# Kernel optimization log

Measured on AMD Instinct MI355X. Metric: run time of the kernel, lower is better.

The kernel has to match this reference:

```python
import jax, jax.numpy as jnp
import numpy as np

N_NODES = 100000
N_EDGES = 3200000
IN_CH = 128
HID_CH = 128   # 2 * out_channels
OUT_CH = 64


def setup_inputs() -> dict:
    key = jax.random.key(0)
    ks = jax.random.split(key, 6)
    x = jax.random.normal(ks[0], (N_NODES, IN_CH), dtype=jnp.float32)
    edge_index = jax.random.randint(ks[1], (2, N_EDGES), 0, N_NODES, dtype=jnp.int64)
    # Glorot-ish init for GCN linear weights
    W1 = jax.random.normal(ks[2], (IN_CH, HID_CH), dtype=jnp.float32) / np.sqrt(IN_CH)
    b1 = jnp.zeros((HID_CH,), dtype=jnp.float32)
    W2 = jax.random.normal(ks[3], (HID_CH, OUT_CH), dtype=jnp.float32) / np.sqrt(HID_CH)
    b2 = jnp.zeros((OUT_CH,), dtype=jnp.float32)
    return {"x": x, "edge_index": edge_index, "W1": W1, "b1": b1, "W2": W2, "b2": b2}


def gcn_conv(x, src, dst, W, b, n):
    """PyG GCNConv: add self-loops, symmetric D^-1/2 (A+I) D^-1/2 normalization,
    linear transform, scatter-add aggregation, then bias."""
    h = x @ W  # [N, C_out]
    ones = jnp.ones(src.shape[0], dtype=x.dtype)
    deg = jax.ops.segment_sum(ones, dst, num_segments=n) + 1.0  # self-loop degree
    dinv = jax.lax.rsqrt(deg)  # [N]
    coef = dinv[src] * dinv[dst]  # [E] edge normalization
    agg = jax.ops.segment_sum(h[src] * coef[:, None], dst, num_segments=n)
    agg = agg + h * (dinv * dinv)[:, None]  # self-loop contribution
    return agg + b


def reference(x, edge_index, W1, b1, W2, b2):
    src, dst = edge_index[0], edge_index[1]
    n = x.shape[0]
    h = jax.nn.relu(gcn_conv(x, src, dst, W1, b1, n))
    out = jax.nn.relu(gcn_conv(h, src, dst, W2, b2, n))
    return out
```

## Files before the change

kernel.cpp:

```cpp
#include <hip/hip_runtime.h>
#include <hip/hip_fp16.h>
#include <cstdint>
#include <cstddef>


#define BSHIFT 8
#define CAP    12288

typedef _Float16 half8 __attribute__((ext_vector_type(8)));
typedef float f32x4 __attribute__((ext_vector_type(4)));

__global__ __launch_bounds__(256) void k_binit(int* __restrict__ bktcur, int nbkt) {
  int b = blockIdx.x * 256 + threadIdx.x;
  if (b < nbkt) bktcur[b] = b * CAP;
}

__global__ __launch_bounds__(256) void k_part3(const int* __restrict__ src,
                                               const int* __restrict__ dst,
                                               int* __restrict__ bktcur,
                                               int* __restrict__ part, int E,
                                               int nbkt) {
  __shared__ int vals[4096];
  __shared__ unsigned short bid[4096];
  __shared__ int hist[512];
  __shared__ int lbase[512];
  __shared__ int gbase[512];
  const int tid = threadIdx.x;
  const int e0 = blockIdx.x * 4096;
  const int ecnt = min(4096, E - e0);
  for (int b = tid; b < nbkt; b += 256) hist[b] = 0;
  __syncthreads();

  int eb[16], ev[16];
#pragma unroll
  for (int j = 0; j < 16; ++j) {
    const int e = e0 + j * 256 + tid;
    eb[j] = -1;
    ev[j] = 0;
    if (e < E) {
      const int d = dst[e];
      eb[j] = d >> BSHIFT;
      ev[j] = (src[e] << BSHIFT) | (d & ((1 << BSHIFT) - 1));
      atomicAdd(&hist[eb[j]], 1);
    }
  }
  __syncthreads();

  if (tid == 0) {
    int run = 0;
    for (int b = 0; b < nbkt; ++b) {
      const int c = hist[b];
      lbase[b] = run;
      run += c;
    }
  }
  __syncthreads();
  for (int b = tid; b < nbkt; b += 256) {
    const int c = hist[b];
    gbase[b] = c ? atomicAdd(&bktcur[b], c) : 0;
    hist[b] = lbase[b];
  }
  __syncthreads();

#pragma unroll
  for (int j = 0; j < 16; ++j) {
    if (eb[j] >= 0) {
      const int lpos = atomicAdd(&hist[eb[j]], 1);
      vals[lpos] = ev[j];
      bid[lpos] = (unsigned short)eb[j];
    }
  }
  __syncthreads();

  for (int s = tid; s < ecnt; s += 256) {
    const int b = bid[s];
    const int gpos = gbase[b] + (s - lbase[b]);
    if (gpos < (b + 1) * CAP)
      part[gpos] = vals[s];
  }
}

__global__ __launch_bounds__(256) void k_bktscan(const int* __restrict__ bktcur,
                                                 int* __restrict__ bktbase,
                                                 int* __restrict__ offsets, int n,
                                                 int E, int nbkt) {
  __shared__ int sc[512];
  const int t = threadIdx.x;
  sc[t] = (t < nbkt) ? (bktcur[t] - t * CAP) : 0;
  sc[256 + t] = (256 + t < nbkt) ? (bktcur[256 + t] - (256 + t) * CAP) : 0;
  __syncthreads();
  if (t == 0) {
    int run = 0;
    for (int b = 0; b < nbkt; ++b) {
      const int c = sc[b];
      sc[b] = run;
      run += c;
    }
    offsets[n] = E;
    bktbase[nbkt] = E;
  }
  __syncthreads();
  if (t < nbkt) bktbase[t] = sc[t];
  if (256 + t < nbkt) bktbase[256 + t] = sc[256 + t];
}

__global__ __launch_bounds__(256) void k_csr2(const int* __restrict__ part,
                                              const int* __restrict__ bktcur,
                                              const int* __restrict__ bktbase,
                                              int* __restrict__ offsets,
                                              int* __restrict__ csr_src,
                                              float* __restrict__ dinv, int n) {
  __shared__ int cnt[256];
  __shared__ int ts[256];
  const int b = blockIdx.x;
  const int node0 = b << BSHIFT;
  const int nn = min(256, n - node0);
  const int t = threadIdx.x;
  cnt[t] = 0;
  __syncthreads();
  const int w0p = b * CAP;
  const int w1p = min(bktcur[b], w0p + CAP);
  for (int e = w0p + t; e < w1p; e += 256)
    atomicAdd(&cnt[part[e] & ((1 << BSHIFT) - 1)], 1);
  __syncthreads();
  const int c = cnt[t];
  ts[t] = c;
  __syncthreads();
  for (int off = 1; off < 256; off <<= 1) {
    const int u = (t >= off) ? ts[t - off] : 0;
    __syncthreads();
    ts[t] += u;
    __syncthreads();
  }
  const int excl = ts[t] - c;
  const int w0 = bktbase[b];
  if (t < nn) {
    offsets[node0 + t] = w0 + excl;
    dinv[node0 + t] = rsqrtf((float)c + 1.0f);
  }
  cnt[t] = w0 + excl;
  __syncthreads();
  for (int e = w0p + t; e < w1p; e += 256) {
    const int p = part[e];
    const int pos = atomicAdd(&cnt[p & ((1 << BSHIFT) - 1)], 1);
    csr_src[pos] = p >> BSHIFT;
  }
}

template <typename TA, int COLS>
__global__ __launch_bounds__(256) void k_gemm_mfma(const TA* __restrict__ A,
                                                   const float* __restrict__ W,
                                                   const float* __restrict__ dinv,
                                                   __half* __restrict__ Hout,
                                                   int N, int ntiles) {
  constexpr int RW = (COLS == 128) ? 2 : 4;
  constexpr int RPT = RW * 16;
  __shared__ _Float16 Wt[128 * COLS];
  __shared__ _Float16 Lb[4][16][72];
  const int tid = threadIdx.x;
  const int w = tid >> 6;
  const int l = tid & 63;

  for (int f = tid; f < (128 * COLS) / 4; f += 256) {
    const int k = f / (COLS / 4);
    const int c4 = (f % (COLS / 4)) * 4;
    const float4 wv = *reinterpret_cast<const float4*>(W + (size_t)k * COLS + c4);
#pragma unroll
    for (int j = 0; j < 4; ++j) {
      const int cc = c4 + j;
      Wt[(cc * 128 + k) ^ ((cc & 7) << 3)] = (_Float16)(&wv.x)[j];
    }
  }
  __syncthreads();

  const int colw = (COLS == 128) ? (w >> 1) * 64 : 0;
  const int rw = (COLS == 128) ? (w & 1) : w;
  const int koff = (l >> 4) * 8;

  half8 bf[4][4];
#pragma unroll
  for (int t = 0; t < 4; ++t)
#pragma unroll
    for (int s = 0; s < 4; ++s) {
      const int cc = colw + 16 * t + (l & 15);
      const int kk = 32 * s + koff;
      bf[t][s] =
          *reinterpret_cast<const half8*>(&Wt[(cc * 128 + kk) ^ ((cc & 7) << 3)]);
    }

  for (int tile = blockIdx.x; tile < ntiles; tile += gridDim.x) {
    const int row = tile * RPT + rw * 16 + (l & 15);
    const int rowc = (row < N) ? row : (N - 1);
    f32x4 acc[4];
#pragma unroll
    for (int t = 0; t < 4; ++t) acc[t] = (f32x4){0.f, 0.f, 0.f, 0.f};

#pragma unroll
    for (int s = 0; s < 4; ++s) {
      half8 af;
      if constexpr (sizeof(TA) == 4) {
        const float* ap = (const float*)A + (size_t)rowc * 128 + 32 * s + koff;
        const float4 a0 = *reinterpret_cast<const float4*>(ap);
        const float4 a1 = *reinterpret_cast<const float4*>(ap + 4);
#pragma unroll
        for (int j = 0; j < 4; ++j) {
          af[j] = (_Float16)(&a0.x)[j];
          af[4 + j] = (_Float16)(&a1.x)[j];
        }
      } else {
        af = *reinterpret_cast<const half8*>((const __half*)A +
                                             (size_t)rowc * 128 + 32 * s + koff);
      }
#pragma unroll
      for (int t = 0; t < 4; ++t)
        acc[t] = __builtin_amdgcn_mfma_f32_16x16x32_f16(af, bf[t][s], acc[t],
                                                        0, 0, 0);
    }

    const int rbase = tile * RPT + rw * 16 + (l >> 4) * 4;
    float dr[4];
#pragma unroll
    for (int r = 0; r < 4; ++r) {
      const int rr = rbase + r;
      dr[r] = (rr < N) ? dinv[rr] : 0.f;
    }

#pragma unroll
    for (int t = 0; t < 4; ++t)
#pragma unroll
      for (int r = 0; r < 4; ++r)
        Lb[w][(l >> 4) * 4 + r][16 * t + (l & 15)] = (_Float16)(acc[t][r] * dr[r]);
    const int orow = tile * RPT + rw * 16 + (l & 15);
    if (orow < N) {
      const int ch = (l >> 4) * 16;
      const half8 v0 = *reinterpret_cast<const half8*>(&Lb[w][l & 15][ch]);
      const half8 v1 = *reinterpret_cast<const half8*>(&Lb[w][l & 15][ch + 8]);
      __half* hp = Hout + (size_t)orow * COLS + colw + ch;
      *reinterpret_cast<half8*>(hp) = v0;
      *reinterpret_cast<half8*>(hp + 8) = v1;
    }
  }
}

__global__ __launch_bounds__(256) void k_gather128(
    const __half* __restrict__ H, const int* __restrict__ offsets,
    const int* __restrict__ csr_src, const float* __restrict__ dinv,
    const float* __restrict__ bias, __half* __restrict__ out, int N) {
  const int lane = threadIdx.x & 63;
  const int g = lane >> 3;
  const int sl = lane & 7;
  int w = (blockIdx.x * 256 + threadIdx.x) >> 6;
  const int nw = (gridDim.x * 256) >> 6;
  for (int i = w; i < N; i += nw) {
    const int beg = offsets[i];
    const int end = offsets[i + 1];
    float acc[16];
    {
      const float vf = (g == 0) ? 1.f : 0.f;
      const float4 ha = *reinterpret_cast<const float4*>(H + (size_t)i * 128 + sl * 16);
      const float4 hb = *reinterpret_cast<const float4*>(H + (size_t)i * 128 + sl * 16 + 8);
      const __half2* pa = reinterpret_cast<const __half2*>(&ha);
      const __half2* pb = reinterpret_cast<const __half2*>(&hb);
#pragma unroll
      for (int q = 0; q < 4; ++q) {
        const float2 fa = __half22float2(pa[q]);
        const float2 fb = __half22float2(pb[q]);
        acc[q * 2] = vf * fa.x;
        acc[q * 2 + 1] = vf * fa.y;
        acc[8 + q * 2] = vf * fb.x;
        acc[8 + q * 2 + 1] = vf * fb.y;
      }
    }
    int base = beg;
    for (; base + 16 <= end; base += 16) {
      const int s0 = __builtin_nontemporal_load(csr_src + base + g);
      const int s1 = __builtin_nontemporal_load(csr_src + base + 8 + g);
      const float4 h0a = *reinterpret_cast<const float4*>(H + (size_t)s0 * 128 + sl * 16);
      const float4 h0b = *reinterpret_cast<const float4*>(H + (size_t)s0 * 128 + sl * 16 + 8);
      const float4 h1a = *reinterpret_cast<const float4*>(H + (size_t)s1 * 128 + sl * 16);
      const float4 h1b = *reinterpret_cast<const float4*>(H + (size_t)s1 * 128 + sl * 16 + 8);
      const __half2* p0a = reinterpret_cast<const __half2*>(&h0a);
      const __half2* p0b = reinterpret_cast<const __half2*>(&h0b);
      const __half2* p1a = reinterpret_cast<const __half2*>(&h1a);
      const __half2* p1b = reinterpret_cast<const __half2*>(&h1b);
#pragma unroll
      for (int q = 0; q < 4; ++q) {
        const float2 f0a = __half22float2(p0a[q]);
        const float2 f0b = __half22float2(p0b[q]);
        const float2 f1a = __half22float2(p1a[q]);
        const float2 f1b = __half22float2(p1b[q]);
        acc[q * 2] += f0a.x + f1a.x;
        acc[q * 2 + 1] += f0a.y + f1a.y;
        acc[8 + q * 2] += f0b.x + f1b.x;
        acc[8 + q * 2 + 1] += f0b.y + f1b.y;
      }
    }
    for (; base < end; base += 8) {
      const int e = base + g;
      const bool v = e < end;
      const int s = v ? __builtin_nontemporal_load(csr_src + e) : i;
      const float vf = v ? 1.f : 0.f;
      const float4 ha = *reinterpret_cast<const float4*>(H + (size_t)s * 128 + sl * 16);
      const float4 hb = *reinterpret_cast<const float4*>(H + (size_t)s * 128 + sl * 16 + 8);
      const __half2* pa = reinterpret_cast<const __half2*>(&ha);
      const __half2* pb = reinterpret_cast<const __half2*>(&hb);
#pragma unroll
      for (int q = 0; q < 4; ++q) {
        const float2 fa = __half22float2(pa[q]);
        const float2 fb = __half22float2(pb[q]);
        acc[q * 2] = fmaf(vf, fa.x, acc[q * 2]);
        acc[q * 2 + 1] = fmaf(vf, fa.y, acc[q * 2 + 1]);
        acc[8 + q * 2] = fmaf(vf, fb.x, acc[8 + q * 2]);
        acc[8 + q * 2 + 1] = fmaf(vf, fb.y, acc[8 + q * 2 + 1]);
      }
    }
#pragma unroll
    for (int j = 0; j < 16; ++j) {
      float a = acc[j];
      a += __shfl_xor(a, 8);
      a += __shfl_xor(a, 16);
      a += __shfl_xor(a, 32);
      acc[j] = a;
    }
    if (g == 0) {
      const float di = dinv[i];
      __half2 ov[8];
#pragma unroll
      for (int q = 0; q < 8; ++q) {
        const float2 bv = *reinterpret_cast<const float2*>(bias + sl * 16 + q * 2);
        ov[q] = __floats2half2_rn(fmaxf(fmaf(di, acc[q * 2], bv.x), 0.f),
                                  fmaxf(fmaf(di, acc[q * 2 + 1], bv.y), 0.f));
      }
      __half* op = out + (size_t)i * 128 + sl * 16;
      *reinterpret_cast<float4*>(op) = *reinterpret_cast<const float4*>(&ov[0]);
      *reinterpret_cast<float4*>(op + 8) = *reinterpret_cast<const float4*>(&ov[4]);
    }
  }
}

__global__ __launch_bounds__(256) void k_gather64(
    const __half* __restrict__ H, const int* __restrict__ offsets,
    const int* __restrict__ csr_src, const float* __restrict__ dinv,
    const float* __restrict__ bias, float* __restrict__ out, int N) {
  const int lane = threadIdx.x & 63;
  const int g = lane >> 3;
  const int sl = lane & 7;
  int w = (blockIdx.x * 256 + threadIdx.x) >> 6;
  const int nw = (gridDim.x * 256) >> 6;
  for (int i = w; i < N; i += nw) {
    const int beg = offsets[i];
    const int end = offsets[i + 1];
    float acc[8];
    {
      const float vf = (g == 0) ? 1.f : 0.f;
      const float4 ha = *reinterpret_cast<const float4*>(H + (size_t)i * 64 + sl * 8);
      const __half2* pa = reinterpret_cast<const __half2*>(&ha);
#pragma unroll
      for (int q = 0; q < 4; ++q) {
        const float2 fa = __half22float2(pa[q]);
        acc[q * 2] = vf * fa.x;
        acc[q * 2 + 1] = vf * fa.y;
      }
    }
    int base = beg;
    for (; base + 16 <= end; base += 16) {
      const int s0 = __builtin_nontemporal_load(csr_src + base + g);
      const int s1 = __builtin_nontemporal_load(csr_src + base + 8 + g);
      const float4 h0 = *reinterpret_cast<const float4*>(H + (size_t)s0 * 64 + sl * 8);
      const float4 h1 = *reinterpret_cast<const float4*>(H + (size_t)s1 * 64 + sl * 8);
      const __half2* p0 = reinterpret_cast<const __half2*>(&h0);
      const __half2* p1 = reinterpret_cast<const __half2*>(&h1);
#pragma unroll
      for (int q = 0; q < 4; ++q) {
        const float2 f0 = __half22float2(p0[q]);
        const float2 f1 = __half22float2(p1[q]);
        acc[q * 2] += f0.x + f1.x;
        acc[q * 2 + 1] += f0.y + f1.y;
      }
    }
    for (; base < end; base += 8) {
      const int e = base + g;
      const bool v = e < end;
      const int s = v ? __builtin_nontemporal_load(csr_src + e) : i;
      const float vf = v ? 1.f : 0.f;
      const float4 ha = *reinterpret_cast<const float4*>(H + (size_t)s * 64 + sl * 8);
      const __half2* pa = reinterpret_cast<const __half2*>(&ha);
#pragma unroll
      for (int q = 0; q < 4; ++q) {
        const float2 fa = __half22float2(pa[q]);
        acc[q * 2] = fmaf(vf, fa.x, acc[q * 2]);
        acc[q * 2 + 1] = fmaf(vf, fa.y, acc[q * 2 + 1]);
      }
    }
#pragma unroll
    for (int j = 0; j < 8; ++j) {
      float a = acc[j];
      a += __shfl_xor(a, 8);
      a += __shfl_xor(a, 16);
      a += __shfl_xor(a, 32);
      acc[j] = a;
    }
    if (g == 0) {
      const float di = dinv[i];
      float* op = out + (size_t)i * 64 + sl * 8;
      const float4 b0 = *reinterpret_cast<const float4*>(bias + sl * 8);
      const float4 b1 = *reinterpret_cast<const float4*>(bias + sl * 8 + 4);
      float4 o;
      o.x = fmaxf(fmaf(di, acc[0], b0.x), 0.f);
      o.y = fmaxf(fmaf(di, acc[1], b0.y), 0.f);
      o.z = fmaxf(fmaf(di, acc[2], b0.z), 0.f);
      o.w = fmaxf(fmaf(di, acc[3], b0.w), 0.f);
      *reinterpret_cast<float4*>(op) = o;
      o.x = fmaxf(fmaf(di, acc[4], b1.x), 0.f);
      o.y = fmaxf(fmaf(di, acc[5], b1.y), 0.f);
      o.z = fmaxf(fmaf(di, acc[6], b1.z), 0.f);
      o.w = fmaxf(fmaf(di, acc[7], b1.w), 0.f);
      *reinterpret_cast<float4*>(op + 4) = o;
    }
  }
}

extern "C" void kernel_launch(void* const* d_in, const int* in_sizes, int n_in,
                              void* d_out, int out_size, void* d_ws,
                              size_t ws_size, hipStream_t stream) {
  const float* x  = (const float*)d_in[0];
  const int*   ei = (const int*)d_in[1];
  const float* W1 = (const float*)d_in[2];
  const float* b1 = (const float*)d_in[3];
  const float* W2 = (const float*)d_in[4];
  const float* b2 = (const float*)d_in[5];

  const int IN  = 128;
  const int n   = in_sizes[0] / IN;
  const int E   = in_sizes[1] / 2;
  const int* srcv = ei;
  const int* dstv = ei + E;
  float* out = (float*)d_out;

  const int NBKT = (n + 255) >> BSHIFT;
  const int NCHK = (E + 4095) / 4096;
  const int NT1  = (n + 31) / 32;
  const int NT2  = (n + 63) / 64;

  char* p = (char*)d_ws;
  auto take = [&](size_t bytes) {
    char* r = p;
    p += (bytes + 255) & ~(size_t)255;
    return r;
  };
  float*  dinv    = (float*)take((size_t)n * 4);
  int*    offsets = (int*)take((size_t)(n + 1) * 4);
  int*    bktbase = (int*)take(512 * 4);
  int*    bktcur  = (int*)take(512 * 4);
  int*    csr_src = (int*)take((size_t)E * 4);
  __half* H16     = (__half*)take((size_t)n * 128 * 2);
  __half* hprime  = (__half*)take((size_t)n * 128 * 2);
  int*    part    = (int*)hprime;

  k_binit<<<(NBKT + 255) / 256, 256, 0, stream>>>(bktcur, NBKT);
  k_part3<<<NCHK, 256, 0, stream>>>(srcv, dstv, bktcur, part, E, NBKT);
  k_bktscan<<<1, 256, 0, stream>>>(bktcur, bktbase, offsets, n, E, NBKT);
  k_csr2<<<NBKT, 256, 0, stream>>>(part, bktcur, bktbase, offsets, csr_src,
                                   dinv, n);

  k_gemm_mfma<float, 128><<<512, 256, 0, stream>>>(x, W1, dinv, H16, n, NT1);
  k_gather128<<<25000, 256, 0, stream>>>(H16, offsets, csr_src, dinv, b1,
                                         hprime, n);

  k_gemm_mfma<__half, 64><<<512, 256, 0, stream>>>(hprime, W2, dinv, H16, n, NT2);
  k_gather64<<<25000, 256, 0, stream>>>(H16, offsets, csr_src, dinv, b2,
                                        out, n);
}
```

Baseline: 298.6 us.

## Fuse bucket scan into CSR build, stage window in LDS, unroll gathers by 32

```diff
diff --git a/kernel.cpp b/kernel.cpp
--- a/kernel.cpp
+++ b/kernel.cpp
@@ -80,48 +80,38 @@
   }
 }
 
-__global__ __launch_bounds__(256) void k_bktscan(const int* __restrict__ bktcur,
-                                                 int* __restrict__ bktbase,
-                                                 int* __restrict__ offsets, int n,
-                                                 int E, int nbkt) {
-  __shared__ int sc[512];
-  const int t = threadIdx.x;
-  sc[t] = (t < nbkt) ? (bktcur[t] - t * CAP) : 0;
-  sc[256 + t] = (256 + t < nbkt) ? (bktcur[256 + t] - (256 + t) * CAP) : 0;
-  __syncthreads();
-  if (t == 0) {
-    int run = 0;
-    for (int b = 0; b < nbkt; ++b) {
-      const int c = sc[b];
-      sc[b] = run;
-      run += c;
-    }
-    offsets[n] = E;
-    bktbase[nbkt] = E;
-  }
-  __syncthreads();
-  if (t < nbkt) bktbase[t] = sc[t];
-  if (256 + t < nbkt) bktbase[256 + t] = sc[256 + t];
-}
-
-__global__ __launch_bounds__(256) void k_csr2(const int* __restrict__ part,
+__global__ __launch_bounds__(256) void k_csr3(const int* __restrict__ part,
                                               const int* __restrict__ bktcur,
-                                              const int* __restrict__ bktbase,
                                               int* __restrict__ offsets,
                                               int* __restrict__ csr_src,
-                                              float* __restrict__ dinv, int n) {
+                                              float* __restrict__ dinv, int n,
+                                              int E) {
+  __shared__ int win[CAP];
   __shared__ int cnt[256];
   __shared__ int ts[256];
   const int b = blockIdx.x;
   const int node0 = b << BSHIFT;
   const int nn = min(256, n - node0);
   const int t = threadIdx.x;
+
+  int partial = 0;
+  for (int j = t; j < b; j += 256) partial += bktcur[j] - j * CAP;
+  ts[t] = partial;
+  __syncthreads();
+  for (int off = 128; off > 0; off >>= 1) {
+    if (t < off) ts[t] += ts[t + off];
+    __syncthreads();
+  }
+  const int w0 = ts[0];
+  __syncthreads();
+
+  const int w0p = b * CAP;
+  const int wcnt = min(bktcur[b], w0p + CAP) - w0p;
+  for (int e = t; e < wcnt; e += 256) win[e] = part[w0p + e];
   cnt[t] = 0;
   __syncthreads();
-  const int w0p = b * CAP;
-  const int w1p = min(bktcur[b], w0p + CAP);
-  for (int e = w0p + t; e < w1p; e += 256)
-    atomicAdd(&cnt[part[e] & ((1 << BSHIFT) - 1)], 1);
+  for (int e = t; e < wcnt; e += 256)
+    atomicAdd(&cnt[win[e] & ((1 << BSHIFT) - 1)], 1);
   __syncthreads();
   const int c = cnt[t];
   ts[t] = c;
@@ -133,15 +123,15 @@
     __syncthreads();
   }
   const int excl = ts[t] - c;
-  const int w0 = bktbase[b];
   if (t < nn) {
     offsets[node0 + t] = w0 + excl;
     dinv[node0 + t] = rsqrtf((float)c + 1.0f);
   }
+  if (b == 0 && t == 0) offsets[n] = E;
   cnt[t] = w0 + excl;
   __syncthreads();
-  for (int e = w0p + t; e < w1p; e += 256) {
-    const int p = part[e];
+  for (int e = t; e < wcnt; e += 256) {
+    const int p = win[e];
     const int pos = atomicAdd(&cnt[p & ((1 << BSHIFT) - 1)], 1);
     csr_src[pos] = p >> BSHIFT;
   }
@@ -272,6 +262,33 @@
       }
     }
     int base = beg;
+    for (; base + 32 <= end; base += 32) {
+      int s[4];
+#pragma unroll
+      for (int u = 0; u < 4; ++u)
+        s[u] = __builtin_nontemporal_load(csr_src + base + u * 8 + g);
+      float4 hv[8];
+#pragma unroll
+      for (int u = 0; u < 4; ++u) {
+        hv[u * 2] = *reinterpret_cast<const float4*>(H + (size_t)s[u] * 128 + sl * 16);
+        hv[u * 2 + 1] =
+            *reinterpret_cast<const float4*>(H + (size_t)s[u] * 128 + sl * 16 + 8);
+      }
+#pragma unroll
+      for (int u = 0; u < 4; ++u) {
+        const __half2* pa = reinterpret_cast<const __half2*>(&hv[u * 2]);
+        const __half2* pb = reinterpret_cast<const __half2*>(&hv[u * 2 + 1]);
+#pragma unroll
+        for (int q = 0; q < 4; ++q) {
+          const float2 fa = __half22float2(pa[q]);
+          const float2 fb = __half22float2(pb[q]);
+          acc[q * 2] += fa.x;
+          acc[q * 2 + 1] += fa.y;
+          acc[8 + q * 2] += fb.x;
+          acc[8 + q * 2 + 1] += fb.y;
+        }
+      }
+    }
     for (; base + 16 <= end; base += 16) {
       const int s0 = __builtin_nontemporal_load(csr_src + base + g);
       const int s1 = __builtin_nontemporal_load(csr_src + base + 8 + g);
@@ -363,6 +380,26 @@
       }
     }
     int base = beg;
+    for (; base + 32 <= end; base += 32) {
+      int s[4];
+#pragma unroll
+      for (int u = 0; u < 4; ++u)
+        s[u] = __builtin_nontemporal_load(csr_src + base + u * 8 + g);
+      float4 hv[4];
+#pragma unroll
+      for (int u = 0; u < 4; ++u)
+        hv[u] = *reinterpret_cast<const float4*>(H + (size_t)s[u] * 64 + sl * 8);
+#pragma unroll
+      for (int u = 0; u < 4; ++u) {
+        const __half2* pa = reinterpret_cast<const __half2*>(&hv[u]);
+#pragma unroll
+        for (int q = 0; q < 4; ++q) {
+          const float2 fa = __half22float2(pa[q]);
+          acc[q * 2] += fa.x;
+          acc[q * 2 + 1] += fa.y;
+        }
+      }
+    }
     for (; base + 16 <= end; base += 16) {
       const int s0 = __builtin_nontemporal_load(csr_src + base + g);
       const int s1 = __builtin_nontemporal_load(csr_src + base + 8 + g);
@@ -450,7 +487,6 @@
   };
   float*  dinv    = (float*)take((size_t)n * 4);
   int*    offsets = (int*)take((size_t)(n + 1) * 4);
-  int*    bktbase = (int*)take(512 * 4);
   int*    bktcur  = (int*)take(512 * 4);
   int*    csr_src = (int*)take((size_t)E * 4);
   __half* H16     = (__half*)take((size_t)n * 128 * 2);
@@ -459,9 +495,7 @@
 
   k_binit<<<(NBKT + 255) / 256, 256, 0, stream>>>(bktcur, NBKT);
   k_part3<<<NCHK, 256, 0, stream>>>(srcv, dstv, bktcur, part, E, NBKT);
-  k_bktscan<<<1, 256, 0, stream>>>(bktcur, bktbase, offsets, n, E, NBKT);
-  k_csr2<<<NBKT, 256, 0, stream>>>(part, bktcur, bktbase, offsets, csr_src,
-                                   dinv, n);
+  k_csr3<<<NBKT, 256, 0, stream>>>(part, bktcur, offsets, csr_src, dinv, n, E);
 
   k_gemm_mfma<float, 128><<<512, 256, 0, stream>>>(x, W1, dinv, H16, n, NT1);
   k_gather128<<<25000, 256, 0, stream>>>(H16, offsets, csr_src, dinv, b1,
```

Measured after the change: 301.6 us. No clear change (+1.0%).
